# Kernel optimization log

Hardware: AMD Instinct MI355X
Metric: run time of the kernel (lower is better)

## Reference

```python
import jax, jax.numpy as jnp
import numpy as np

WS = 7   # window size
SS = 3   # shift size
NH = 3   # num heads


def _rel_pos_index(ws):
    # [N, N] int index into (2*ws-1)^2 bias table, N = ws*ws
    coords = np.stack(np.meshgrid(np.arange(ws), np.arange(ws), indexing='ij')).reshape(2, -1)
    rel = coords[:, :, None] - coords[:, None, :]
    rel = rel.transpose(1, 2, 0).copy()
    rel[..., 0] += ws - 1
    rel[..., 1] += ws - 1
    rel[..., 0] *= 2 * ws - 1
    return rel.sum(-1)


def _attn_mask(H, W, ws, ss):
    # [nW, N, N] additive mask (0 / -1e9) for shifted windows
    img = np.zeros((H, W))
    cnt = 0
    slices = (slice(0, -ws), slice(-ws, -ss), slice(-ss, None))
    for h in slices:
        for w in slices:
            img[h, w] = cnt
            cnt += 1
    img = np.roll(img, (-ss, -ss), axis=(0, 1))
    mw = img.reshape(H // ws, ws, W // ws, ws).transpose(0, 2, 1, 3).reshape(-1, ws * ws)
    d = mw[:, None, :] - mw[:, :, None]
    return np.where(d != 0, -1e9, 0.0).astype(np.float32)


def setup_inputs() -> dict:
    key = jax.random.key(0)
    ks = jax.random.split(key, 6)
    B, H, W, C = 32, 112, 112, 96
    return {
        'x': jax.random.normal(ks[0], (B, H, W, C), jnp.float32),
        'qkv_w': jax.random.normal(ks[1], (C, 3 * C), jnp.float32) * 0.02,
        'qkv_b': jax.random.normal(ks[2], (3 * C,), jnp.float32) * 0.02,
        'proj_w': jax.random.normal(ks[3], (C, C), jnp.float32) * 0.02,
        'proj_b': jax.random.normal(ks[4], (C,), jnp.float32) * 0.02,
        'bias_table': jax.random.normal(ks[5], ((2 * WS - 1) ** 2, NH), jnp.float32) * 0.02,
    }


def reference(x, qkv_w, qkv_b, proj_w, proj_b, bias_table):
    B, H, W, C = x.shape
    ws, ss, nh = WS, SS, NH
    hd = C // nh
    scale = hd ** -0.5
    N = ws * ws
    # cyclic shift
    x = jnp.roll(x, (-ss, -ss), axis=(1, 2))
    # window partition -> [BnW, N, C]
    xw = x.reshape(B, H // ws, ws, W // ws, ws, C).transpose(0, 1, 3, 2, 4, 5).reshape(-1, N, C)
    BnW = xw.shape[0]
    qkv = (xw @ qkv_w + qkv_b).reshape(BnW, N, 3, nh, hd).transpose(2, 0, 3, 1, 4)
    q, k, v = qkv[0] * scale, qkv[1], qkv[2]  # [BnW, nh, N, hd]
    attn = jnp.einsum('bhnd,bhmd->bhnm', q, k)
    # relative position bias: gather [N*N] rows -> [nh, N, N]
    rel_idx = jnp.asarray(_rel_pos_index(ws))
    bias = bias_table[rel_idx.reshape(-1)].reshape(N, N, nh).transpose(2, 0, 1)
    attn = attn + bias[None]
    # shifted-window mask
    mask = jnp.asarray(_attn_mask(H, W, ws, ss))  # [nW, N, N]
    nW = mask.shape[0]
    attn = (attn.reshape(-1, nW, nh, N, N) + mask[None, :, None]).reshape(BnW, nh, N, N)
    attn = jax.nn.softmax(attn, axis=-1)
    out = jnp.einsum('bhnm,bhmd->bhnd', attn, v).transpose(0, 2, 1, 3).reshape(BnW, N, C)
    out = out @ proj_w + proj_b
    # window reverse + reverse shift
    xo = out.reshape(B, H // ws, W // ws, ws, ws, C).transpose(0, 1, 3, 2, 4, 5).reshape(B, H, W, C)
    return jnp.roll(xo, (ss, ss), axis=(1, 2))
```

## Files before the change

### kernel.cpp

```cpp
#include <hip/hip_runtime.h>

typedef __bf16 bf16x2 __attribute__((ext_vector_type(2)));
typedef __bf16 bf16x4 __attribute__((ext_vector_type(4)));
typedef __bf16 bf16x8 __attribute__((ext_vector_type(8)));
typedef float  f32x4  __attribute__((ext_vector_type(4)));

#define QKV_PACK_ELEMS 27648
#define PROJ_PACK_ELEMS 9216
#define TOTAL_PACK (QKV_PACK_ELEMS + PROJ_PACK_ELEMS)
#define BM_ELEMS (9 * 3 * 49 * 64)

#define LOG2E 1.4426950408889634f
#define QSCALE (0.17677669529663687f * 1.4426950408889634f)

__device__ __forceinline__ float fexp2(float x) {
    float r; asm("v_exp_f32 %0, %1" : "=v"(r) : "v"(x)); return r;
}

__device__ __forceinline__ int region1(int g) {
    return (g < 105) ? 0 : ((g < 109) ? 1 : 2);
}

__global__ __launch_bounds__(256) void prepack(
    const float* __restrict__ qkvw, const float* __restrict__ projw,
    const float* __restrict__ btab, __bf16* __restrict__ wp)
{
    int t = blockIdx.x * 256 + threadIdx.x;
    if (t < QKV_PACK_ELEMS) {
        int j = t & 7, lane = (t >> 3) & 63, g = t >> 9;
        int nt = g / 3, ks = g - 3 * nt;
        int k = ks * 32 + (lane >> 4) * 8 + j;
        int c = nt * 16 + (lane & 15);
        wp[t] = (__bf16)qkvw[k * 288 + c];
    } else if (t < TOTAL_PACK) {
        int t2 = t - QKV_PACK_ELEMS;
        int j = t2 & 7, lane = (t2 >> 3) & 63, g = t2 >> 9;
        int nt = g / 3, ks = g - 3 * nt;
        int k = ks * 32 + (lane >> 4) * 8 + j;
        int c = nt * 16 + (lane & 15);
        wp[t] = (__bf16)projw[k * 96 + c];
    } else if (t < TOTAL_PACK + BM_ELEMS) {
        int t2 = t - TOTAL_PACK;
        int k  = t2 & 63;
        int r  = t2 >> 6;
        int q  = r % 49;
        int r2 = r / 49;
        int h  = r2 % 3;
        int cls = r2 / 3;
        int rowcls = cls / 3, colcls = cls % 3;
        int wy = (rowcls == 0) ? 0 : (rowcls == 1 ? 14 : 15);
        int wx = (colcls == 0) ? 0 : (colcls == 1 ? 14 : 15);
        float val = -1e9f;
        if (k < 49) {
            int qi = q / 7, qj = q % 7, ki = k / 7, kj = k % 7;
            int rq = region1((wy * 7 + qi + 3) % 112) * 3 + region1((wx * 7 + qj + 3) % 112);
            int rk = region1((wy * 7 + ki + 3) % 112) * 3 + region1((wx * 7 + kj + 3) % 112);
            if (rq == rk)
                val = btab[((qi - ki + 6) * 13 + (qj - kj + 6)) * 3 + h] * LOG2E;
        }
        wp[TOTAL_PACK + t2] = (__bf16)val;
    }
}

__global__ __launch_bounds__(256, 4) void swmsa_fused(
    const float* __restrict__ xg,
    const __bf16* __restrict__ wp,
    const float* __restrict__ qkvb,
    const float* __restrict__ projb,
    float* __restrict__ outg)
{
    __shared__ __align__(16) char smem[40896];
    __bf16* xb  = (__bf16*)smem;
    __bf16* Qb  = (__bf16*)smem;
    __bf16* Pb  = (__bf16*)smem;
    __bf16* Kb  = (__bf16*)(smem + 10192);
    __bf16* Vt  = (__bf16*)(smem + 21952);
    __bf16* Ost = (__bf16*)(smem + 35776);

    const __bf16* wqkv  = wp;
    const __bf16* wproj = wp + QKV_PACK_ELEMS;
    const __bf16* bm    = wp + TOTAL_PACK;

    const int tid  = threadIdx.x;
    const int lane = tid & 63;
    const int wv   = tid >> 6;
    const int quad = lane >> 4;
    const int l16  = lane & 15;

    const int bw   = blockIdx.x;
    const int b    = bw >> 8;
    const int widx = bw & 255;
    const int wy   = widx >> 4, wx = widx & 15;
    const int h0   = wy * 7, w0 = wx * 7;

    for (int idx = tid; idx < 1176; idx += 256) {
        int n  = idx / 24;
        int c4 = idx - n * 24;
        int i = n / 7, j = n - 7 * i;
        int ho = h0 + i + 3; if (ho >= 112) ho -= 112;
        int wo = w0 + j + 3; if (wo >= 112) wo -= 112;
        const float4 v = *(const float4*)(xg + (size_t)((b * 112 + ho) * 112 + wo) * 96 + c4 * 4);
        bf16x4 p; p[0] = (__bf16)v.x; p[1] = (__bf16)v.y; p[2] = (__bf16)v.z; p[3] = (__bf16)v.w;
        *(bf16x4*)(xb + n * 104 + c4 * 4) = p;
    }
    __syncthreads();

    {
        bf16x8 afr[4][3];
        #pragma unroll
        for (int mt = 0; mt < 4; mt++) {
            int row = mt * 16 + l16; if (row > 48) row = 48;
            #pragma unroll
            for (int ks = 0; ks < 3; ks++)
                afr[mt][ks] = *(const bf16x8*)(xb + row * 104 + ks * 32 + quad * 8);
        }

        int nt = wv;
        bf16x8 b0 = *(const bf16x8*)(wqkv + ((nt * 3 + 0) << 9) + (lane << 3));
        bf16x8 b1 = *(const bf16x8*)(wqkv + ((nt * 3 + 1) << 9) + (lane << 3));
        bf16x8 b2 = *(const bf16x8*)(wqkv + ((nt * 3 + 2) << 9) + (lane << 3));
        float4 bias4 = *(const float4*)(qkvb + nt * 16 + quad * 4);
        float  biass = qkvb[nt * 16 + l16];
        __syncthreads();

        while (true) {
            const int ntn = nt + 4;
            const bool more = ntn < 18;
            bf16x8 nb0, nb1, nb2; float4 nbias4; float nbiass = 0.f;
            if (more) {
                nb0 = *(const bf16x8*)(wqkv + ((ntn * 3 + 0) << 9) + (lane << 3));
                nb1 = *(const bf16x8*)(wqkv + ((ntn * 3 + 1) << 9) + (lane << 3));
                nb2 = *(const bf16x8*)(wqkv + ((ntn * 3 + 2) << 9) + (lane << 3));
                nbias4 = *(const float4*)(qkvb + ntn * 16 + quad * 4);
                nbiass = qkvb[ntn * 16 + l16];
            }
            if (nt < 12) {
                #pragma unroll
                for (int mt = 0; mt < 4; mt++) {
                    f32x4 acc = {bias4.x, bias4.y, bias4.z, bias4.w};
                    acc = __builtin_amdgcn_mfma_f32_16x16x32_bf16(b0, afr[mt][0], acc, 0, 0, 0);
                    acc = __builtin_amdgcn_mfma_f32_16x16x32_bf16(b1, afr[mt][1], acc, 0, 0, 0);
                    acc = __builtin_amdgcn_mfma_f32_16x16x32_bf16(b2, afr[mt][2], acc, 0, 0, 0);
                    const int tok = mt * 16 + l16;
                    if (nt < 6) {
                        bf16x4 pk;
                        #pragma unroll
                        for (int r = 0; r < 4; r++) pk[r] = (__bf16)(acc[r] * QSCALE);
                        if (tok < 49)
                            *(bf16x4*)(Qb + tok * 104 + nt * 16 + quad * 4) = pk;
                    } else {
                        bf16x4 pk;
                        #pragma unroll
                        for (int r = 0; r < 4; r++) pk[r] = (__bf16)acc[r];
                        const int hh = (nt - 6) >> 1;
                        const int d0 = ((nt - 6) & 1) * 16;
                        if (tok < 49)
                            *(bf16x4*)(Kb + hh * 1960 + tok * 40 + d0 + quad * 4) = pk;
                    }
                }
            } else {
                const int c = nt * 16 + l16;
                const int cc = c - 192, hh = cc >> 5, d = cc & 31;
                #pragma unroll
                for (int mt = 0; mt < 4; mt++) {
                    f32x4 acc = {biass, biass, biass, biass};
                    acc = __builtin_amdgcn_mfma_f32_16x16x32_bf16(afr[mt][0], b0, acc, 0, 0, 0);
                    acc = __builtin_amdgcn_mfma_f32_16x16x32_bf16(afr[mt][1], b1, acc, 0, 0, 0);
                    acc = __builtin_amdgcn_mfma_f32_16x16x32_bf16(afr[mt][2], b2, acc, 0, 0, 0);
                    const int tokbase = mt * 16 + quad * 4;
                    bf16x4 pk;
                    #pragma unroll
                    for (int r = 0; r < 4; r++) {
                        int tok = tokbase + r;
                        pk[r] = (__bf16)((tok < 49) ? acc[r] : 0.f);
                    }
                    *(bf16x4*)(Vt + hh * 2304 + d * 72 + tokbase) = pk;
                }
            }
            if (!more) break;
            b0 = nb0; b1 = nb1; b2 = nb2; bias4 = nbias4; biass = nbiass; nt = ntn;
        }
    }
    __syncthreads();

    int go[4];
    #pragma unroll
    for (int r = 0; r < 4; r++) {
        int t = 16 * wv + quad * 4 + r; if (t > 48) t = 48;
        int i = t / 7, j = t - 7 * i;
        int ho = h0 + i + 3; if (ho >= 112) ho -= 112;
        int wo = w0 + j + 3; if (wo >= 112) wo -= 112;
        go[r] = ((b * 112 + ho) * 112 + wo) * 96;
    }

    const int cls = ((wy < 14) ? 0 : (wy - 13)) * 3 + ((wx < 14) ? 0 : (wx - 13));
    const int qclamp = (16 * wv + l16 > 48) ? 48 : 16 * wv + l16;
    const __bf16* bmq = bm + ((size_t)(cls * 3) * 49 + qclamp) * 64;

    bf16x8 aq[3];
    #pragma unroll
    for (int h = 0; h < 3; h++)
        aq[h] = *(const bf16x8*)(Qb + qclamp * 104 + h * 32 + quad * 8);
    __syncthreads();

    __bf16* Pw = Pb + wv * 1152;
    __bf16* Ow = Ost + wv * 640;

    f32x4 pacc[6];
    #pragma unroll
    for (int nt = 0; nt < 6; nt++) {
        float pbias = projb[nt * 16 + l16];
        f32x4 t = {pbias, pbias, pbias, pbias};
        pacc[nt] = t;
    }

    #pragma unroll
    for (int h = 0; h < 3; h++) {
        const __bf16* Kh  = Kb + h * 1960;
        const __bf16* bmh = bmq + h * 49 * 64;
        f32x4 S[4];
        bf16x4 bmv[4];
        #pragma unroll
        for (int mt = 0; mt < 4; mt++) {
            int brow = mt * 16 + l16; if (brow > 48) brow = 48;
            bf16x8 bk = *(const bf16x8*)(Kh + brow * 40 + quad * 8);
            f32x4 z = {0.f, 0.f, 0.f, 0.f};
            S[mt] = __builtin_amdgcn_mfma_f32_16x16x32_bf16(bk, aq[h], z, 0, 0, 0);
            bmv[mt] = *(const bf16x4*)(bmh + mt * 16 + quad * 4);
        }
        float e[4][4];
        float sm0 = 0.f, sm1 = 0.f;
        #pragma unroll
        for (int mt = 0; mt < 4; mt++) {
            e[mt][0] = fexp2(S[mt][0] + (float)bmv[mt][0]);
            e[mt][1] = fexp2(S[mt][1] + (float)bmv[mt][1]);
            e[mt][2] = fexp2(S[mt][2] + (float)bmv[mt][2]);
            e[mt][3] = fexp2(S[mt][3] + (float)bmv[mt][3]);
            sm0 += e[mt][0] + e[mt][1];
            sm1 += e[mt][2] + e[mt][3];
        }
        float sm = sm0 + sm1;
        sm += __shfl_xor(sm, 16);
        sm += __shfl_xor(sm, 32);
        float rs = __builtin_amdgcn_rcpf(sm);
        #pragma unroll
        for (int mt = 0; mt < 4; mt++) {
            bf16x4 p;
            p[0] = (__bf16)(e[mt][0] * rs); p[1] = (__bf16)(e[mt][1] * rs);
            p[2] = (__bf16)(e[mt][2] * rs); p[3] = (__bf16)(e[mt][3] * rs);
            *(bf16x4*)(Pw + l16 * 72 + mt * 16 + quad * 4) = p;
        }
        bf16x8 pbf[6];
        #pragma unroll
        for (int nt = 0; nt < 6; nt++)
            pbf[nt] = *(const bf16x8*)(wproj + ((nt * 3 + h) << 9) + (lane << 3));
        {
            const __bf16* Vh = Vt + h * 2304;
            bf16x8 ap0 = *(const bf16x8*)(Pw + l16 * 72 + quad * 8);
            bf16x8 ap1 = *(const bf16x8*)(Pw + l16 * 72 + 32 + quad * 8);
            bf16x8 bv00 = *(const bf16x8*)(Vh + l16 * 72 + quad * 8);
            bf16x8 bv01 = *(const bf16x8*)(Vh + l16 * 72 + 32 + quad * 8);
            bf16x8 bv10 = *(const bf16x8*)(Vh + (16 + l16) * 72 + quad * 8);
            bf16x8 bv11 = *(const bf16x8*)(Vh + (16 + l16) * 72 + 32 + quad * 8);
            f32x4 O0 = {0.f, 0.f, 0.f, 0.f}, O1 = {0.f, 0.f, 0.f, 0.f};
            O0 = __builtin_amdgcn_mfma_f32_16x16x32_bf16(bv00, ap0, O0, 0, 0, 0);
            O0 = __builtin_amdgcn_mfma_f32_16x16x32_bf16(bv01, ap1, O0, 0, 0, 0);
            O1 = __builtin_amdgcn_mfma_f32_16x16x32_bf16(bv10, ap0, O1, 0, 0, 0);
            O1 = __builtin_amdgcn_mfma_f32_16x16x32_bf16(bv11, ap1, O1, 0, 0, 0);
            bf16x4 o0, o1;
            #pragma unroll
            for (int r = 0; r < 4; r++) { o0[r] = (__bf16)O0[r]; o1[r] = (__bf16)O1[r]; }
            *(bf16x4*)(Ow + l16 * 40 + quad * 4)      = o0;
            *(bf16x4*)(Ow + l16 * 40 + 16 + quad * 4) = o1;
            bf16x8 ao = *(const bf16x8*)(Ow + l16 * 40 + quad * 8);
            #pragma unroll
            for (int nt = 0; nt < 6; nt++)
                pacc[nt] = __builtin_amdgcn_mfma_f32_16x16x32_bf16(ao, pbf[nt], pacc[nt], 0, 0, 0);
        }
    }

    #pragma unroll
    for (int nt = 0; nt < 6; nt++) {
        const int c = nt * 16 + l16;
        #pragma unroll
        for (int r = 0; r < 4; r++) {
            int tok = 16 * wv + quad * 4 + r;
            if (tok < 49) outg[go[r] + c] = pacc[nt][r];
        }
    }
}

extern "C" void kernel_launch(void* const* d_in, const int* in_sizes, int n_in,
                              void* d_out, int out_size, void* d_ws, size_t ws_size,
                              hipStream_t stream) {
    const float* xg    = (const float*)d_in[0];
    const float* qkvw  = (const float*)d_in[1];
    const float* qkvb  = (const float*)d_in[2];
    const float* projw = (const float*)d_in[3];
    const float* projb = (const float*)d_in[4];
    const float* btab  = (const float*)d_in[5];
    float* outg = (float*)d_out;
    __bf16* wp = (__bf16*)d_ws;

    prepack<<<dim3((TOTAL_PACK + BM_ELEMS + 255) / 256), dim3(256), 0, stream>>>(
        qkvw, projw, btab, wp);
    swmsa_fused<<<dim3(8192), dim3(256), 0, stream>>>(xg, wp, qkvb, projb, outg);
}
```

Before: 338.7 us.

## Swizzle LDS layouts, shrink shared memory and raise occupancy to 5 blocks

The padded shared-memory rows for X/Q, K, V^T and the per-wave output staging are replaced with unpadded rows that use an XOR swizzle on 8-element groups, so conflict avoidance no longer costs padding. The per-wave O staging buffer now reuses the wave's P buffer, and the total LDS footprint drops from about 40 KB to about 31 KB per block. Launch bounds are raised from 4 to 5 blocks per CU so more windows can be resident at once. The tighter register budget at the higher occupancy target could force spills or reduce instruction scheduling freedom.

```diff
diff --git a/kernel.cpp b/kernel.cpp
--- a/kernel.cpp
+++ b/kernel.cpp
@@ -62,20 +62,19 @@
     }
 }
 
-__global__ __launch_bounds__(256, 4) void swmsa_fused(
+__global__ __launch_bounds__(256, 5) void swmsa_fused(
     const float* __restrict__ xg,
     const __bf16* __restrict__ wp,
     const float* __restrict__ qkvb,
     const float* __restrict__ projb,
     float* __restrict__ outg)
 {
-    __shared__ __align__(16) char smem[40896];
+    __shared__ __align__(16) char smem[31104];
     __bf16* xb  = (__bf16*)smem;
     __bf16* Qb  = (__bf16*)smem;
     __bf16* Pb  = (__bf16*)smem;
-    __bf16* Kb  = (__bf16*)(smem + 10192);
-    __bf16* Vt  = (__bf16*)(smem + 21952);
-    __bf16* Ost = (__bf16*)(smem + 35776);
+    __bf16* Kb  = (__bf16*)(smem + 9408);
+    __bf16* Vt  = (__bf16*)(smem + 18816);
 
     const __bf16* wqkv  = wp;
     const __bf16* wproj = wp + QKV_PACK_ELEMS;
@@ -101,7 +100,7 @@
         int wo = w0 + j + 3; if (wo >= 112) wo -= 112;
         const float4 v = *(const float4*)(xg + (size_t)((b * 112 + ho) * 112 + wo) * 96 + c4 * 4);
         bf16x4 p; p[0] = (__bf16)v.x; p[1] = (__bf16)v.y; p[2] = (__bf16)v.z; p[3] = (__bf16)v.w;
-        *(bf16x4*)(xb + n * 104 + c4 * 4) = p;
+        *(bf16x4*)(xb + ((n * 96 + c4 * 4) ^ ((n & 3) << 3))) = p;
     }
     __syncthreads();
 
@@ -112,7 +111,7 @@
             int row = mt * 16 + l16; if (row > 48) row = 48;
             #pragma unroll
             for (int ks = 0; ks < 3; ks++)
-                afr[mt][ks] = *(const bf16x8*)(xb + row * 104 + ks * 32 + quad * 8);
+                afr[mt][ks] = *(const bf16x8*)(xb + ((row * 96 + ks * 32 + quad * 8) ^ ((row & 3) << 3)));
         }
 
         int nt = wv;
@@ -147,7 +146,7 @@
                         #pragma unroll
                         for (int r = 0; r < 4; r++) pk[r] = (__bf16)(acc[r] * QSCALE);
                         if (tok < 49)
-                            *(bf16x4*)(Qb + tok * 104 + nt * 16 + quad * 4) = pk;
+                            *(bf16x4*)(Qb + ((tok * 96 + nt * 16 + quad * 4) ^ ((tok & 3) << 3))) = pk;
                     } else {
                         bf16x4 pk;
                         #pragma unroll
@@ -155,7 +154,7 @@
                         const int hh = (nt - 6) >> 1;
                         const int d0 = ((nt - 6) & 1) * 16;
                         if (tok < 49)
-                            *(bf16x4*)(Kb + hh * 1960 + tok * 40 + d0 + quad * 4) = pk;
+                            *(bf16x4*)(Kb + hh * 1568 + ((tok * 32 + d0 + quad * 4) ^ ((tok & 3) << 3))) = pk;
                     }
                 }
             } else {
@@ -174,7 +173,7 @@
                         int tok = tokbase + r;
                         pk[r] = (__bf16)((tok < 49) ? acc[r] : 0.f);
                     }
-                    *(bf16x4*)(Vt + hh * 2304 + d * 72 + tokbase) = pk;
+                    *(bf16x4*)(Vt + hh * 2048 + ((d * 64 + tokbase) ^ ((d & 7) << 3))) = pk;
                 }
             }
             if (!more) break;
@@ -200,11 +199,11 @@
     bf16x8 aq[3];
     #pragma unroll
     for (int h = 0; h < 3; h++)
-        aq[h] = *(const bf16x8*)(Qb + qclamp * 104 + h * 32 + quad * 8);
+        aq[h] = *(const bf16x8*)(Qb + ((qclamp * 96 + h * 32 + quad * 8) ^ ((qclamp & 3) << 3)));
     __syncthreads();
 
     __bf16* Pw = Pb + wv * 1152;
-    __bf16* Ow = Ost + wv * 640;
+    __bf16* Ow = Pw;
 
     f32x4 pacc[6];
     #pragma unroll
@@ -216,14 +215,14 @@
 
     #pragma unroll
     for (int h = 0; h < 3; h++) {
-        const __bf16* Kh  = Kb + h * 1960;
+        const __bf16* Kh  = Kb + h * 1568;
         const __bf16* bmh = bmq + h * 49 * 64;
         f32x4 S[4];
         bf16x4 bmv[4];
         #pragma unroll
         for (int mt = 0; mt < 4; mt++) {
             int brow = mt * 16 + l16; if (brow > 48) brow = 48;
-            bf16x8 bk = *(const bf16x8*)(Kh + brow * 40 + quad * 8);
+            bf16x8 bk = *(const bf16x8*)(Kh + ((brow * 32 + quad * 8) ^ ((brow & 3) << 3)));
             f32x4 z = {0.f, 0.f, 0.f, 0.f};
             S[mt] = __builtin_amdgcn_mfma_f32_16x16x32_bf16(bk, aq[h], z, 0, 0, 0);
             bmv[mt] = *(const bf16x4*)(bmh + mt * 16 + quad * 4);
@@ -255,24 +254,26 @@
         for (int nt = 0; nt < 6; nt++)
             pbf[nt] = *(const bf16x8*)(wproj + ((nt * 3 + h) << 9) + (lane << 3));
         {
-            const __bf16* Vh = Vt + h * 2304;
+            const __bf16* Vh = Vt + h * 2048;
             bf16x8 ap0 = *(const bf16x8*)(Pw + l16 * 72 + quad * 8);
             bf16x8 ap1 = *(const bf16x8*)(Pw + l16 * 72 + 32 + quad * 8);
-            bf16x8 bv00 = *(const bf16x8*)(Vh + l16 * 72 + quad * 8);
-            bf16x8 bv01 = *(const bf16x8*)(Vh + l16 * 72 + 32 + quad * 8);
-            bf16x8 bv10 = *(const bf16x8*)(Vh + (16 + l16) * 72 + quad * 8);
-            bf16x8 bv11 = *(const bf16x8*)(Vh + (16 + l16) * 72 + 32 + quad * 8);
+            const int vsw = (l16 & 7) << 3;
+            bf16x8 bv00 = *(const bf16x8*)(Vh + ((l16 * 64 + quad * 8) ^ vsw));
+            bf16x8 bv01 = *(const bf16x8*)(Vh + ((l16 * 64 + 32 + quad * 8) ^ vsw));
+            bf16x8 bv10 = *(const bf16x8*)(Vh + (((16 + l16) * 64 + quad * 8) ^ vsw));
+            bf16x8 bv11 = *(const bf16x8*)(Vh + (((16 + l16) * 64 + 32 + quad * 8) ^ vsw));
             f32x4 O0 = {0.f, 0.f, 0.f, 0.f}, O1 = {0.f, 0.f, 0.f, 0.f};
             O0 = __builtin_amdgcn_mfma_f32_16x16x32_bf16(bv00, ap0, O0, 0, 0, 0);
             O0 = __builtin_amdgcn_mfma_f32_16x16x32_bf16(bv01, ap1, O0, 0, 0, 0);
             O1 = __builtin_amdgcn_mfma_f32_16x16x32_bf16(bv10, ap0, O1, 0, 0, 0);
             O1 = __builtin_amdgcn_mfma_f32_16x16x32_bf16(bv11, ap1, O1, 0, 0, 0);
+            const int osw = (l16 & 3) << 3;
             bf16x4 o0, o1;
             #pragma unroll
             for (int r = 0; r < 4; r++) { o0[r] = (__bf16)O0[r]; o1[r] = (__bf16)O1[r]; }
-            *(bf16x4*)(Ow + l16 * 40 + quad * 4)      = o0;
-            *(bf16x4*)(Ow + l16 * 40 + 16 + quad * 4) = o1;
-            bf16x8 ao = *(const bf16x8*)(Ow + l16 * 40 + quad * 8);
+            *(bf16x4*)(Ow + ((l16 * 32 + quad * 4) ^ osw))      = o0;
+            *(bf16x4*)(Ow + ((l16 * 32 + 16 + quad * 4) ^ osw)) = o1;
+            bf16x8 ao = *(const bf16x8*)(Ow + ((l16 * 32 + quad * 8) ^ osw));
             #pragma unroll
             for (int nt = 0; nt < 6; nt++)
                 pacc[nt] = __builtin_amdgcn_mfma_f32_16x16x32_bf16(ao, pbf[nt], pacc[nt], 0, 0, 0);
```

Result: slower. 476.7 us (+40.8%).
